# Kernel tuning notes

Measured on AMD Instinct MI355X. Metric: run time of the kernel, lower is better.

Reference implementation:

```python
import jax, jax.numpy as jnp
import numpy as np

N, L = 4096, 512

def setup_inputs() -> dict:
    key = jax.random.key(0)
    ks = jax.random.split(key, 12)
    def w(k, shape, fan_in):
        return jax.random.normal(k, shape, jnp.float32) / np.sqrt(fan_in)
    inp = {
        'samples': jax.random.normal(ks[0], (N, 1, L), jnp.float32),
        'samples_info': jax.random.randint(ks[1], (N, 2), 0, 2).astype(jnp.int64),
        'conv1_w': w(ks[2], (64, 1, 100), 100),
        'conv1_b': jnp.zeros((64,), jnp.float32),
        'conv2_w': w(ks[3], (128, 64, 5), 64 * 5),
        'conv2_b': jnp.zeros((128,), jnp.float32),
        'conv3_w': w(ks[4], (256, 128, 3), 128 * 3),
        'conv3_b': jnp.zeros((256,), jnp.float32),
        'fc_w': w(ks[5], (128, 256), 256),
        'fc_b': jnp.zeros((128,), jnp.float32),
        'bn_gamma': jnp.ones((128,), jnp.float32),
        'bn_beta': jnp.zeros((128,), jnp.float32),
        'bn_mean': jnp.zeros((128,), jnp.float32),
        'bn_var': jnp.ones((128,), jnp.float32),
    }
    return inp

def _conv1d(x, w, b, pad):
    # x: [N,C,L], w: [O,C,K]; torch padding='same' for k=100 pads (49,50)
    y = jax.lax.conv_general_dilated(x, w, window_strides=(1,), padding=[pad],
                                     dimension_numbers=('NCH', 'OIH', 'NCH'))
    return y + b[None, :, None]

def _maxpool2(x):
    n, c, l = x.shape
    return x.reshape(n, c, l // 2, 2).max(-1)

def reference(samples, samples_info, conv1_w, conv1_b, conv2_w, conv2_b,
              conv3_w, conv3_b, fc_w, fc_b, bn_gamma, bn_beta, bn_mean, bn_var):
    h = _maxpool2(jax.nn.relu(_conv1d(samples, conv1_w, conv1_b, (49, 50))))
    h = _maxpool2(jax.nn.relu(_conv1d(h, conv2_w, conv2_b, (2, 2))))
    h = _maxpool2(jax.nn.relu(_conv1d(h, conv3_w, conv3_b, (1, 1))))
    h = h.mean(-1)                                  # AdaptiveAvgPool1d(1)+Flatten -> [N,256]
    h = jax.nn.relu(h @ fc_w.T + fc_b)              # Linear 256->128
    z = bn_gamma * (h - bn_mean) * jax.lax.rsqrt(bn_var + 1e-5) + bn_beta  # BN (eval)
    # all-pairs euclidean distances via the cdist identity (replaces N^2 python loop)
    sq = jnp.sum(z * z, axis=-1)
    d2 = sq[:, None] + sq[None, :] - 2.0 * (z @ z.T)
    n = z.shape[0]
    offdiag = ~jnp.eye(n, dtype=bool)
    d = jnp.sqrt(jnp.where(offdiag, jnp.maximum(d2, 0.0), 1.0))
    writer = samples_info[:, 0]
    gen = samples_info[:, 1]
    y = ((writer[:, None] == writer[None, :]) & (gen[:, None] == 1) & (gen[None, :] == 1)).astype(z.dtype)
    cl = jnp.where(offdiag, y * d + (1.0 - y) * jax.nn.relu(1.0 - d), 0.0)
    return cl  # [N,N] contrastive loss per ordered pair (i!=j); diagonal masked to 0
```

## Files before the change

### kernel.cpp

```cpp
#include <hip/hip_runtime.h>
#include <math.h>

#define NS 4096

typedef _Float16 half8 __attribute__((ext_vector_type(8)));
typedef _Float16 half2v __attribute__((ext_vector_type(2)));
typedef float floatx16 __attribute__((ext_vector_type(16)));

#define P1T_OFF     0
#define P1T_STRIDE  72
#define P2T_OFF     9360
#define P2T_STRIDE  136
#define XC_OFF      9360
#define XC_STRIDE   648
#define SCR_OFF     1024
#define B1_OFF      18200
#define B2_OFF      18264
#define B3_OFF      18392
#define PR_OFF      18648
#define LDS_MAIN_FLOATS 19288

__global__ void prep_weights(const float* __restrict__ w1,
                             const float* __restrict__ w2,
                             const float* __restrict__ w3,
                             _Float16* __restrict__ w1p,
                             _Float16* __restrict__ w2p,
                             _Float16* __restrict__ w3p)
{
    int gid = blockIdx.x * 256 + threadIdx.x;
    if (gid < 8192) {
        int m = gid >> 7, k = gid & 127;
        w1p[gid] = (k < 100) ? (_Float16)w1[m * 100 + k] : (_Float16)0.f;
    } else if (gid < 49152) {
        int r = gid - 8192;
        int dk = r >> 13, rem = r & 8191;
        int m = rem >> 6, i = rem & 63;
        w2p[r] = (_Float16)w2[(m * 64 + i) * 5 + dk];
    } else if (gid < 147456) {
        int r = gid - 49152;
        int dk = r >> 15, rem = r & 32767;
        int m = rem >> 7, i = rem & 127;
        w3p[r] = (_Float16)w3[(m * 128 + i) * 3 + dk];
    }
}

__device__ __forceinline__ float dpp_rowsum16(float v) {
    int x;
    x = __builtin_amdgcn_update_dpp(0, __float_as_int(v), 0x111, 0xF, 0xF, true);
    v += __int_as_float(x);
    x = __builtin_amdgcn_update_dpp(0, __float_as_int(v), 0x112, 0xF, 0xF, true);
    v += __int_as_float(x);
    x = __builtin_amdgcn_update_dpp(0, __float_as_int(v), 0x114, 0xF, 0xF, true);
    v += __int_as_float(x);
    x = __builtin_amdgcn_update_dpp(0, __float_as_int(v), 0x118, 0xF, 0xF, true);
    v += __int_as_float(x);
    return v;
}


__global__ __launch_bounds__(512, 4)
void cnn_fused(const float* __restrict__ samples, const int* __restrict__ info,
               const _Float16* __restrict__ w1p,
               const _Float16* __restrict__ w2p,
               const _Float16* __restrict__ w3p,
               const float* __restrict__ b1, const float* __restrict__ b2,
               const float* __restrict__ b3,
               const float* __restrict__ fcw, const float* __restrict__ fcb,
               const float* __restrict__ gamma_, const float* __restrict__ beta_,
               const float* __restrict__ bnm, const float* __restrict__ bnv,
               _Float16* __restrict__ zh, float* __restrict__ sqout,
               int* __restrict__ uout)
{
    extern __shared__ float lds[];
    _Float16* p1T = (_Float16*)(lds + P1T_OFF);
    _Float16* p2T = (_Float16*)(lds + P2T_OFF);
    _Float16* xc  = (_Float16*)(lds + XC_OFF);

    const int n    = blockIdx.x;
    const int t    = threadIdx.x;
    const int lane = t & 63;
    const int wave = t >> 6;
    const int g    = lane >> 5;
    const int col  = lane & 31;

    {
        const float* sp = samples + n * 512;
        const int c = wave;
        for (int u = lane; u < XC_STRIDE; u += 64) {
            int src = u + c - 49;
            xc[c * XC_STRIDE + u] = (_Float16)((src >= 0 && src < 512) ? sp[src] : 0.f);
        }
    }
    if (t < 64)              lds[B1_OFF + t] = b1[t];
    if (t >= 64 && t < 192)  lds[B2_OFF + (t - 64)] = b2[t - 64];
    if (t >= 192 && t < 448) lds[B3_OFF + (t - 192)] = b3[t - 192];
    for (int i = t; i < 640; i += 512) {
        int k = i & 127;
        const float* p = (i < 128) ? fcb : (i < 256) ? gamma_ : (i < 384) ? beta_
                       : (i < 512) ? bnm : bnv;
        lds[PR_OFF + i] = p[k];
    }
    if (t < 144) {
        int rr = t / 36, c4 = t - rr * 36;
        int row = (rr < 2) ? rr : (256 + rr);
        lds[P1T_OFF + row * 36 + c4] = 0.f;
    }
    if (t == 0) uout[n] = (info[2 * n + 1] == 1) ? info[2 * n] : -1;
    __syncthreads();

    auto pool_store = [&](floatx16& acc, _Float16* dst) {
        float vm[16];
        #pragma unroll
        for (int r = 0; r < 16; ++r) {
            float v = fmaxf(acc[r], 0.f);
            vm[r] = fmaxf(v, __shfl_xor(v, 1));
        }
        if (!(lane & 1)) {
            #pragma unroll
            for (int rq = 0; rq < 4; ++rq) {
                half2v p0, p1;
                p0[0] = (_Float16)vm[4 * rq];     p0[1] = (_Float16)vm[4 * rq + 1];
                p1[0] = (_Float16)vm[4 * rq + 2]; p1[1] = (_Float16)vm[4 * rq + 3];
                *(half2v*)(dst + 8 * rq)     = p0;
                *(half2v*)(dst + 8 * rq + 2) = p1;
            }
        }
    };

    {
        const int mt   = wave >> 2;
        const int ntb1 = (wave & 3) * 4;
        half8 A[7];
        #pragma unroll
        for (int kb = 0; kb < 7; ++kb)
            A[kb] = *(const half8*)(w1p + (mt * 32 + col) * 128 + kb * 16 + g * 8);
        float4 bq[4];
        #pragma unroll
        for (int q4 = 0; q4 < 4; ++q4)
            bq[q4] = *(const float4*)&lds[B1_OFF + mt * 32 + 8 * q4 + 4 * g];
        #pragma unroll
        for (int s = 0; s < 4; ++s) {
            const int nt = ntb1 + s;
            const int nn = nt * 32 + col;
            const int c  = nn & 7;
            const _Float16* xcp = xc + c * XC_STRIDE + (nn - c) + g * 8;
            floatx16 a;
            #pragma unroll
            for (int q4 = 0; q4 < 4; ++q4) {
                a[4 * q4 + 0] = bq[q4].x; a[4 * q4 + 1] = bq[q4].y;
                a[4 * q4 + 2] = bq[q4].z; a[4 * q4 + 3] = bq[q4].w;
            }
            #pragma unroll
            for (int kb = 0; kb < 7; ++kb) {
                half8 B = *(const half8*)(xcp + kb * 16);
                a = __builtin_amdgcn_mfma_f32_32x32x16_f16(A[kb], B, a, 0, 0, 0);
            }
            const int P = 2 + nt * 16 + (col >> 1);
            pool_store(a, p1T + P * P1T_STRIDE + mt * 32 + 4 * g);
        }
    }
    __syncthreads();

    {
        if (t < 136) {
            int row = (t < 68) ? 0 : 129;
            int c4 = (t < 68) ? t : (t - 68);
            lds[P2T_OFF + row * 68 + c4] = 0.f;
        }
        const int mt  = wave & 3;
        const int ntb = (wave >> 2) * 4;
        floatx16 acc[4];
        #pragma unroll
        for (int q4 = 0; q4 < 4; ++q4) {
            float4 bq = *(const float4*)&lds[B2_OFF + mt * 32 + 8 * q4 + 4 * g];
            #pragma unroll
            for (int s = 0; s < 4; ++s) {
                acc[s][4 * q4 + 0] = bq.x; acc[s][4 * q4 + 1] = bq.y;
                acc[s][4 * q4 + 2] = bq.z; acc[s][4 * q4 + 3] = bq.w;
            }
        }
        half8 Ac[4], An[4];
        #pragma unroll
        for (int kb = 0; kb < 4; ++kb)
            Ac[kb] = *(const half8*)(w2p + (mt * 32 + col) * 64 + kb * 16 + g * 8);
        #pragma unroll 1
        for (int dk = 0; dk < 5; ++dk) {
            if (dk < 4) {
                #pragma unroll
                for (int kb = 0; kb < 4; ++kb)
                    An[kb] = *(const half8*)(w2p + ((dk + 1) * 128 + mt * 32 + col) * 64 + kb * 16 + g * 8);
            }
            #pragma unroll
            for (int s = 0; s < 4; ++s) {
                const int row = (ntb + s) * 32 + col + dk;
                const _Float16* bp = p1T + row * P1T_STRIDE + g * 8;
                #pragma unroll
                for (int kb = 0; kb < 4; ++kb) {
                    half8 B = *(const half8*)(bp + kb * 16);
                    acc[s] = __builtin_amdgcn_mfma_f32_32x32x16_f16(Ac[kb], B, acc[s], 0, 0, 0);
                }
            }
            if (dk < 4) {
                #pragma unroll
                for (int kb = 0; kb < 4; ++kb) Ac[kb] = An[kb];
            }
        }
        #pragma unroll
        for (int s = 0; s < 4; ++s) {
            const int P = 1 + (ntb + s) * 16 + (col >> 1);
            pool_store(acc[s], p2T + P * P2T_STRIDE + mt * 32 + 4 * g);
        }
    }
    __syncthreads();

    {
        const int mt = wave;
        floatx16 acc[4];
        #pragma unroll
        for (int q4 = 0; q4 < 4; ++q4) {
            float4 bq = *(const float4*)&lds[B3_OFF + mt * 32 + 8 * q4 + 4 * g];
            #pragma unroll
            for (int s = 0; s < 4; ++s) {
                acc[s][4 * q4 + 0] = bq.x; acc[s][4 * q4 + 1] = bq.y;
                acc[s][4 * q4 + 2] = bq.z; acc[s][4 * q4 + 3] = bq.w;
            }
        }
        #pragma unroll 1
        for (int dk = 0; dk < 3; ++dk) {
            half8 A[8];
            #pragma unroll
            for (int kb = 0; kb < 8; ++kb)
                A[kb] = *(const half8*)(w3p + (dk * 256 + mt * 32 + col) * 128 + kb * 16 + g * 8);
            #pragma unroll
            for (int s = 0; s < 4; ++s) {
                const int row = s * 32 + col + dk;
                const _Float16* bp = p2T + row * P2T_STRIDE + g * 8;
                #pragma unroll
                for (int kb = 0; kb < 8; ++kb) {
                    half8 B = *(const half8*)(bp + kb * 16);
                    acc[s] = __builtin_amdgcn_mfma_f32_32x32x16_f16(A[kb], B, acc[s], 0, 0, 0);
                }
            }
        }
        #pragma unroll
        for (int r = 0; r < 16; ++r) {
            float srow = 0.f;
            #pragma unroll
            for (int s = 0; s < 4; ++s) {
                float v = fmaxf(acc[s][r], 0.f);
                srow += fmaxf(v, __shfl_xor(v, 1));
            }
            float s16 = dpp_rowsum16(srow);
            float s32 = s16 + __shfl_xor(s16, 16);
            if ((lane & 31) == 15) {
                int ch = mt * 32 + (r & 3) + 8 * (r >> 2) + 4 * g;
                lds[SCR_OFF + ch] = s32 * (1.f / 128.f);
            }
        }
    }
    __syncthreads();

    {
        const float4 xv = *(const float4*)&lds[SCR_OFF + 4 * lane];
        #pragma unroll 1
        for (int ow = 0; ow < 16; ow += 4) {
            const int o0 = wave * 16 + ow;
            const float4 w0 = *(const float4*)&fcw[(o0 + 0) * 256 + 4 * lane];
            const float4 w1 = *(const float4*)&fcw[(o0 + 1) * 256 + 4 * lane];
            const float4 w2 = *(const float4*)&fcw[(o0 + 2) * 256 + 4 * lane];
            const float4 w3 = *(const float4*)&fcw[(o0 + 3) * 256 + 4 * lane];
            float s0 = w0.x * xv.x + w0.y * xv.y + w0.z * xv.z + w0.w * xv.w;
            float s1 = w1.x * xv.x + w1.y * xv.y + w1.z * xv.z + w1.w * xv.w;
            float s2 = w2.x * xv.x + w2.y * xv.y + w2.z * xv.z + w2.w * xv.w;
            float s3 = w3.x * xv.x + w3.y * xv.y + w3.z * xv.z + w3.w * xv.w;
            #pragma unroll
            for (int off = 32; off > 0; off >>= 1) {
                s0 += __shfl_down(s0, off);
                s1 += __shfl_down(s1, off);
                s2 += __shfl_down(s2, off);
                s3 += __shfl_down(s3, off);
            }
            if (lane == 0) {
                float4 o;
                o.x = fmaxf(s0 + lds[PR_OFF + o0 + 0], 0.f);
                o.y = fmaxf(s1 + lds[PR_OFF + o0 + 1], 0.f);
                o.z = fmaxf(s2 + lds[PR_OFF + o0 + 2], 0.f);
                o.w = fmaxf(s3 + lds[PR_OFF + o0 + 3], 0.f);
                *(float4*)&lds[SCR_OFF + 256 + o0] = o;
            }
        }
    }
    __syncthreads();

    if (t < 128) {
        float hv = lds[SCR_OFF + 256 + t];
        float zv = lds[PR_OFF + 128 + t] * (hv - lds[PR_OFF + 384 + t])
                   * (1.f / sqrtf(lds[PR_OFF + 512 + t] + 1e-5f)) + lds[PR_OFF + 256 + t];
        _Float16 zq = (_Float16)zv;
        zh[(size_t)n * 128 + t] = zq;
        float zqf = (float)zq;
        lds[SCR_OFF + 384 + t] = zqf * zqf;
    }
    __syncthreads();
    if (t < 64) {
        float s = lds[SCR_OFF + 384 + t] + lds[SCR_OFF + 384 + 64 + t];
        #pragma unroll
        for (int off = 32; off > 0; off >>= 1) s += __shfl_down(s, off);
        if (t == 0) sqout[n] = s;
    }
}

#define PW_STRIDE 136
#define PW_LDS_BYTES (2 * 128 * PW_STRIDE * 2)

__global__ __launch_bounds__(256, 2)
void pairwise_mfma(const _Float16* __restrict__ zh, const float* __restrict__ sq,
                   const int* __restrict__ u, float* __restrict__ out)
{
    extern __shared__ float ldsf[];
    _Float16* at = (_Float16*)ldsf;
    _Float16* bt = at + 128 * PW_STRIDE;
    const int t = threadIdx.x;
    const int i0 = blockIdx.y * 128;
    const int j0 = blockIdx.x * 128;

    #pragma unroll
    for (int r4 = 0; r4 < 8; ++r4) {
        int idx = t + 256 * r4;
        int row = idx >> 4, c8 = (idx & 15) * 8;
        *(half8*)(at + row * PW_STRIDE + c8) = *(const half8*)(zh + (size_t)(i0 + row) * 128 + c8);
        *(half8*)(bt + row * PW_STRIDE + c8) = *(const half8*)(zh + (size_t)(j0 + row) * 128 + c8);
    }
    __syncthreads();

    const int lane = t & 63, wave = t >> 6;
    const int g = lane >> 5, col = lane & 31;
    const int ib = (wave & 1) * 64, jb = (wave >> 1) * 64;

    half8 A[2][8];
    #pragma unroll
    for (int mt = 0; mt < 2; ++mt)
        #pragma unroll
        for (int kb = 0; kb < 8; ++kb)
            A[mt][kb] = *(const half8*)(at + (ib + mt * 32 + col) * PW_STRIDE + kb * 16 + g * 8);

    floatx16 acc[2][2];
    #pragma unroll
    for (int a = 0; a < 2; ++a)
        #pragma unroll
        for (int b = 0; b < 2; ++b)
            #pragma unroll
            for (int r = 0; r < 16; ++r) acc[a][b][r] = 0.f;

    #pragma unroll
    for (int nt = 0; nt < 2; ++nt)
        #pragma unroll
        for (int kb = 0; kb < 8; ++kb) {
            half8 B = *(const half8*)(bt + (jb + nt * 32 + col) * PW_STRIDE + kb * 16 + g * 8);
            acc[0][nt] = __builtin_amdgcn_mfma_f32_32x32x16_f16(A[0][kb], B, acc[0][nt], 0, 0, 0);
            acc[1][nt] = __builtin_amdgcn_mfma_f32_32x32x16_f16(A[1][kb], B, acc[1][nt], 0, 0, 0);
        }

    #pragma unroll
    for (int nt = 0; nt < 2; ++nt) {
        const int j = j0 + jb + nt * 32 + col;
        const float sqj = sq[j];
        const int uj = u[j];
        #pragma unroll
        for (int mt = 0; mt < 2; ++mt) {
            #pragma unroll
            for (int r = 0; r < 16; ++r) {
                const int i = i0 + ib + mt * 32 + (r & 3) + 8 * (r >> 2) + 4 * g;
                float res;
                if (i == j) {
                    res = 0.f;
                } else {
                    float d2 = sq[i] + sqj - 2.f * acc[mt][nt][r];
                    float d = sqrtf(fmaxf(d2, 0.f));
                    int ui = u[i];
                    res = (ui == uj && ui >= 0) ? d : fmaxf(1.f - d, 0.f);
                }
                out[(size_t)i * 4096 + j] = res;
            }
        }
    }
}

extern "C" void kernel_launch(void* const* d_in, const int* in_sizes, int n_in,
                              void* d_out, int out_size, void* d_ws, size_t ws_size,
                              hipStream_t stream)
{
    const float* samples = (const float*)d_in[0];
    const int*   info    = (const int*)d_in[1];
    const float* w1  = (const float*)d_in[2];
    const float* b1  = (const float*)d_in[3];
    const float* w2  = (const float*)d_in[4];
    const float* b2  = (const float*)d_in[5];
    const float* w3  = (const float*)d_in[6];
    const float* b3  = (const float*)d_in[7];
    const float* fcw = (const float*)d_in[8];
    const float* fcb = (const float*)d_in[9];
    const float* g   = (const float*)d_in[10];
    const float* be  = (const float*)d_in[11];
    const float* bm  = (const float*)d_in[12];
    const float* bv  = (const float*)d_in[13];
    float* out = (float*)d_out;

    _Float16* zhws = (_Float16*)d_ws;
    float*    sqws = (float*)((char*)d_ws + (1 << 20));
    int*      uws  = (int*)((char*)d_ws + (1 << 20) + 16384);
    _Float16* wp   = (_Float16*)((char*)d_ws + (1 << 20) + 32768);
    _Float16* w1p = wp;
    _Float16* w2p = wp + 8192;
    _Float16* w3p = wp + 49152;

    hipLaunchKernelGGL(prep_weights, dim3(576), dim3(256), 0, stream,
                       w1, w2, w3, w1p, w2p, w3p);

    hipLaunchKernelGGL(cnn_fused, dim3(NS), dim3(512),
                       LDS_MAIN_FLOATS * sizeof(float), stream,
                       samples, info, w1p, w2p, w3p, b1, b2, b3, fcw, fcb,
                       g, be, bm, bv, zhws, sqws, uws);

    hipLaunchKernelGGL(pairwise_mfma, dim3(32, 32), dim3(256),
                       PW_LDS_BYTES, stream,
                       zhws, sqws, uws, out);
}
```

Measured before the change: 425.4 us.

## Software-pipeline conv MFMA loops, fuse FC/BN epilogue, slim pairwise LDS

The three conv stages are restructured into fully unrolled loops that double/triple-buffer A and B fragments, so loads for step i+1 are issued while MFMAs for step i run, and accumulators are shared across the N tiles. The FC output, BN and fp16 quantization plus the squared norm are fused into the FC reduction lane, which removes two barriers and the LDS round trips between them. The pairwise kernel now reads the A operand straight from global memory instead of staging it in LDS, halving LDS use and raising launch_bounds occupancy to 4. In exchange it uses more registers and makes uncoalesced global reads in the pairwise kernel.

```diff
diff --git a/kernel.cpp b/kernel.cpp
--- a/kernel.cpp
+++ b/kernel.cpp
@@ -130,33 +130,47 @@
     {
         const int mt   = wave >> 2;
         const int ntb1 = (wave & 3) * 4;
-        half8 A[7];
-        #pragma unroll
-        for (int kb = 0; kb < 7; ++kb)
-            A[kb] = *(const half8*)(w1p + (mt * 32 + col) * 128 + kb * 16 + g * 8);
-        float4 bq[4];
-        #pragma unroll
-        for (int q4 = 0; q4 < 4; ++q4)
-            bq[q4] = *(const float4*)&lds[B1_OFF + mt * 32 + 8 * q4 + 4 * g];
+        const _Float16* ap = w1p + (mt * 32 + col) * 128 + g * 8;
+        const _Float16* bps[4];
         #pragma unroll
         for (int s = 0; s < 4; ++s) {
             const int nt = ntb1 + s;
             const int nn = nt * 32 + col;
             const int c  = nn & 7;
-            const _Float16* xcp = xc + c * XC_STRIDE + (nn - c) + g * 8;
-            floatx16 a;
-            #pragma unroll
-            for (int q4 = 0; q4 < 4; ++q4) {
-                a[4 * q4 + 0] = bq[q4].x; a[4 * q4 + 1] = bq[q4].y;
-                a[4 * q4 + 2] = bq[q4].z; a[4 * q4 + 3] = bq[q4].w;
-            }
-            #pragma unroll
-            for (int kb = 0; kb < 7; ++kb) {
-                half8 B = *(const half8*)(xcp + kb * 16);
-                a = __builtin_amdgcn_mfma_f32_32x32x16_f16(A[kb], B, a, 0, 0, 0);
-            }
-            const int P = 2 + nt * 16 + (col >> 1);
-            pool_store(a, p1T + P * P1T_STRIDE + mt * 32 + 4 * g);
+            bps[s] = xc + c * XC_STRIDE + (nn - c) + g * 8;
+        }
+        floatx16 acc[4];
+        #pragma unroll
+        for (int q4 = 0; q4 < 4; ++q4) {
+            float4 bq = *(const float4*)&lds[B1_OFF + mt * 32 + 8 * q4 + 4 * g];
+            #pragma unroll
+            for (int s = 0; s < 4; ++s) {
+                acc[s][4 * q4 + 0] = bq.x; acc[s][4 * q4 + 1] = bq.y;
+                acc[s][4 * q4 + 2] = bq.z; acc[s][4 * q4 + 3] = bq.w;
+            }
+        }
+        half8 Aa[3], Bb[2][4];
+        Aa[0] = *(const half8*)(ap);
+        Aa[1] = *(const half8*)(ap + 16);
+        #pragma unroll
+        for (int s = 0; s < 4; ++s) Bb[0][s] = *(const half8*)(bps[s]);
+        #pragma unroll
+        for (int i = 0; i < 7; ++i) {
+            if (i < 5)
+                Aa[(i + 2) % 3] = *(const half8*)(ap + (i + 2) * 16);
+            if (i < 6) {
+                #pragma unroll
+                for (int s = 0; s < 4; ++s)
+                    Bb[(i + 1) & 1][s] = *(const half8*)(bps[s] + (i + 1) * 16);
+            }
+            #pragma unroll
+            for (int s = 0; s < 4; ++s)
+                acc[s] = __builtin_amdgcn_mfma_f32_32x32x16_f16(Aa[i % 3], Bb[i & 1][s], acc[s], 0, 0, 0);
+        }
+        #pragma unroll
+        for (int s = 0; s < 4; ++s) {
+            const int P = 2 + (ntb1 + s) * 16 + (col >> 1);
+            pool_store(acc[s], p1T + P * P1T_STRIDE + mt * 32 + 4 * g);
         }
     }
     __syncthreads();
@@ -169,6 +183,11 @@
         }
         const int mt  = wave & 3;
         const int ntb = (wave >> 2) * 4;
+        const _Float16* ap = w2p + (mt * 32 + col) * 64 + g * 8;
+        const _Float16* bps[4];
+        #pragma unroll
+        for (int s = 0; s < 4; ++s)
+            bps[s] = p1T + ((ntb + s) * 32 + col) * P1T_STRIDE + g * 8;
         floatx16 acc[4];
         #pragma unroll
         for (int q4 = 0; q4 < 4; ++q4) {
@@ -179,31 +198,26 @@
                 acc[s][4 * q4 + 2] = bq.z; acc[s][4 * q4 + 3] = bq.w;
             }
         }
-        half8 Ac[4], An[4];
-        #pragma unroll
-        for (int kb = 0; kb < 4; ++kb)
-            Ac[kb] = *(const half8*)(w2p + (mt * 32 + col) * 64 + kb * 16 + g * 8);
-        #pragma unroll 1
-        for (int dk = 0; dk < 5; ++dk) {
-            if (dk < 4) {
+        half8 Aa[3], Bb[2][4];
+        Aa[0] = *(const half8*)(ap);
+        Aa[1] = *(const half8*)(ap + 16);
+        #pragma unroll
+        for (int s = 0; s < 4; ++s) Bb[0][s] = *(const half8*)(bps[s]);
+        #pragma unroll
+        for (int i = 0; i < 20; ++i) {
+            if (i < 18) {
+                const int j = i + 2, dkj = j >> 2, kbj = j & 3;
+                Aa[(i + 2) % 3] = *(const half8*)(ap + dkj * 8192 + kbj * 16);
+            }
+            if (i < 19) {
+                const int j = i + 1, dkj = j >> 2, kbj = j & 3;
                 #pragma unroll
-                for (int kb = 0; kb < 4; ++kb)
-                    An[kb] = *(const half8*)(w2p + ((dk + 1) * 128 + mt * 32 + col) * 64 + kb * 16 + g * 8);
-            }
-            #pragma unroll
-            for (int s = 0; s < 4; ++s) {
-                const int row = (ntb + s) * 32 + col + dk;
-                const _Float16* bp = p1T + row * P1T_STRIDE + g * 8;
-                #pragma unroll
-                for (int kb = 0; kb < 4; ++kb) {
-                    half8 B = *(const half8*)(bp + kb * 16);
-                    acc[s] = __builtin_amdgcn_mfma_f32_32x32x16_f16(Ac[kb], B, acc[s], 0, 0, 0);
-                }
-            }
-            if (dk < 4) {
-                #pragma unroll
-                for (int kb = 0; kb < 4; ++kb) Ac[kb] = An[kb];
-            }
+                for (int s = 0; s < 4; ++s)
+                    Bb[j & 1][s] = *(const half8*)(bps[s] + dkj * P1T_STRIDE + kbj * 16);
+            }
+            #pragma unroll
+            for (int s = 0; s < 4; ++s)
+                acc[s] = __builtin_amdgcn_mfma_f32_32x32x16_f16(Aa[i % 3], Bb[i & 1][s], acc[s], 0, 0, 0);
         }
         #pragma unroll
         for (int s = 0; s < 4; ++s) {
@@ -215,6 +229,11 @@
 
     {
         const int mt = wave;
+        const _Float16* ap = w3p + (mt * 32 + col) * 128 + g * 8;
+        const _Float16* bps[4];
+        #pragma unroll
+        for (int s = 0; s < 4; ++s)
+            bps[s] = p2T + (s * 32 + col) * P2T_STRIDE + g * 8;
         floatx16 acc[4];
         #pragma unroll
         for (int q4 = 0; q4 < 4; ++q4) {
@@ -225,22 +244,26 @@
                 acc[s][4 * q4 + 2] = bq.z; acc[s][4 * q4 + 3] = bq.w;
             }
         }
-        #pragma unroll 1
-        for (int dk = 0; dk < 3; ++dk) {
-            half8 A[8];
-            #pragma unroll
-            for (int kb = 0; kb < 8; ++kb)
-                A[kb] = *(const half8*)(w3p + (dk * 256 + mt * 32 + col) * 128 + kb * 16 + g * 8);
-            #pragma unroll
-            for (int s = 0; s < 4; ++s) {
-                const int row = s * 32 + col + dk;
-                const _Float16* bp = p2T + row * P2T_STRIDE + g * 8;
+        half8 Aa[3], Bb[2][4];
+        Aa[0] = *(const half8*)(ap);
+        Aa[1] = *(const half8*)(ap + 16);
+        #pragma unroll
+        for (int s = 0; s < 4; ++s) Bb[0][s] = *(const half8*)(bps[s]);
+        #pragma unroll
+        for (int i = 0; i < 24; ++i) {
+            if (i < 22) {
+                const int j = i + 2, dkj = j >> 3, kbj = j & 7;
+                Aa[(i + 2) % 3] = *(const half8*)(ap + dkj * 32768 + kbj * 16);
+            }
+            if (i < 23) {
+                const int j = i + 1, dkj = j >> 3, kbj = j & 7;
                 #pragma unroll
-                for (int kb = 0; kb < 8; ++kb) {
-                    half8 B = *(const half8*)(bp + kb * 16);
-                    acc[s] = __builtin_amdgcn_mfma_f32_32x32x16_f16(A[kb], B, acc[s], 0, 0, 0);
-                }
-            }
+                for (int s = 0; s < 4; ++s)
+                    Bb[j & 1][s] = *(const half8*)(bps[s] + dkj * P2T_STRIDE + kbj * 16);
+            }
+            #pragma unroll
+            for (int s = 0; s < 4; ++s)
+                acc[s] = __builtin_amdgcn_mfma_f32_32x32x16_f16(Aa[i % 3], Bb[i & 1][s], acc[s], 0, 0, 0);
         }
         #pragma unroll
         for (int r = 0; r < 16; ++r) {
@@ -262,6 +285,7 @@
 
     {
         const float4 xv = *(const float4*)&lds[SCR_OFF + 4 * lane];
+        float sqpart = 0.f;
         #pragma unroll 1
         for (int ow = 0; ow < 16; ow += 4) {
             const int o0 = wave * 16 + ow;
@@ -281,45 +305,43 @@
                 s3 += __shfl_down(s3, off);
             }
             if (lane == 0) {
-                float4 o;
-                o.x = fmaxf(s0 + lds[PR_OFF + o0 + 0], 0.f);
-                o.y = fmaxf(s1 + lds[PR_OFF + o0 + 1], 0.f);
-                o.z = fmaxf(s2 + lds[PR_OFF + o0 + 2], 0.f);
-                o.w = fmaxf(s3 + lds[PR_OFF + o0 + 3], 0.f);
-                *(float4*)&lds[SCR_OFF + 256 + o0] = o;
-            }
-        }
-    }
-    __syncthreads();
-
-    if (t < 128) {
-        float hv = lds[SCR_OFF + 256 + t];
-        float zv = lds[PR_OFF + 128 + t] * (hv - lds[PR_OFF + 384 + t])
-                   * (1.f / sqrtf(lds[PR_OFF + 512 + t] + 1e-5f)) + lds[PR_OFF + 256 + t];
-        _Float16 zq = (_Float16)zv;
-        zh[(size_t)n * 128 + t] = zq;
-        float zqf = (float)zq;
-        lds[SCR_OFF + 384 + t] = zqf * zqf;
-    }
-    __syncthreads();
-    if (t < 64) {
-        float s = lds[SCR_OFF + 384 + t] + lds[SCR_OFF + 384 + 64 + t];
-        #pragma unroll
-        for (int off = 32; off > 0; off >>= 1) s += __shfl_down(s, off);
-        if (t == 0) sqout[n] = s;
+                float sv[4] = {s0, s1, s2, s3};
+                half2v zp0, zp1;
+                #pragma unroll
+                for (int k = 0; k < 4; ++k) {
+                    float hv = fmaxf(sv[k] + lds[PR_OFF + o0 + k], 0.f);
+                    float zv = lds[PR_OFF + 128 + o0 + k] * (hv - lds[PR_OFF + 384 + o0 + k])
+                             * (1.f / sqrtf(lds[PR_OFF + 512 + o0 + k] + 1e-5f))
+                             + lds[PR_OFF + 256 + o0 + k];
+                    _Float16 zq = (_Float16)zv;
+                    if (k < 2) zp0[k] = zq; else zp1[k - 2] = zq;
+                    float zqf = (float)zq;
+                    sqpart += zqf * zqf;
+                }
+                *(half2v*)(zh + (size_t)n * 128 + o0)     = zp0;
+                *(half2v*)(zh + (size_t)n * 128 + o0 + 2) = zp1;
+            }
+        }
+        if (lane == 0) lds[SCR_OFF + 256 + wave] = sqpart;
+    }
+    __syncthreads();
+    if (t == 0) {
+        float s = 0.f;
+        #pragma unroll
+        for (int w = 0; w < 8; ++w) s += lds[SCR_OFF + 256 + w];
+        sqout[n] = s;
     }
 }
 
 #define PW_STRIDE 136
-#define PW_LDS_BYTES (2 * 128 * PW_STRIDE * 2)
-
-__global__ __launch_bounds__(256, 2)
+#define PW_LDS_BYTES (128 * PW_STRIDE * 2)
+
+__global__ __launch_bounds__(256, 4)
 void pairwise_mfma(const _Float16* __restrict__ zh, const float* __restrict__ sq,
                    const int* __restrict__ u, float* __restrict__ out)
 {
     extern __shared__ float ldsf[];
-    _Float16* at = (_Float16*)ldsf;
-    _Float16* bt = at + 128 * PW_STRIDE;
+    _Float16* bt = (_Float16*)ldsf;
     const int t = threadIdx.x;
     const int i0 = blockIdx.y * 128;
     const int j0 = blockIdx.x * 128;
@@ -328,7 +350,6 @@
     for (int r4 = 0; r4 < 8; ++r4) {
         int idx = t + 256 * r4;
         int row = idx >> 4, c8 = (idx & 15) * 8;
-        *(half8*)(at + row * PW_STRIDE + c8) = *(const half8*)(zh + (size_t)(i0 + row) * 128 + c8);
         *(half8*)(bt + row * PW_STRIDE + c8) = *(const half8*)(zh + (size_t)(j0 + row) * 128 + c8);
     }
     __syncthreads();
@@ -337,12 +358,10 @@
     const int g = lane >> 5, col = lane & 31;
     const int ib = (wave & 1) * 64, jb = (wave >> 1) * 64;
 
-    half8 A[2][8];
-    #pragma unroll
-    for (int mt = 0; mt < 2; ++mt)
-        #pragma unroll
-        for (int kb = 0; kb < 8; ++kb)
-            A[mt][kb] = *(const half8*)(at + (ib + mt * 32 + col) * PW_STRIDE + kb * 16 + g * 8);
+    const _Float16* ap0 = zh + (size_t)(i0 + ib + col) * 128 + g * 8;
+    const _Float16* ap1 = zh + (size_t)(i0 + ib + 32 + col) * 128 + g * 8;
+    const _Float16* bp0 = bt + (jb + col) * PW_STRIDE + g * 8;
+    const _Float16* bp1 = bt + (jb + 32 + col) * PW_STRIDE + g * 8;
 
     floatx16 acc[2][2];
     #pragma unroll
@@ -352,14 +371,24 @@
             #pragma unroll
             for (int r = 0; r < 16; ++r) acc[a][b][r] = 0.f;
 
+    half8 A0[2], A1[2], B0[2], B1[2];
+    A0[0] = *(const half8*)(ap0);
+    A1[0] = *(const half8*)(ap1);
+    B0[0] = *(const half8*)(bp0);
+    B1[0] = *(const half8*)(bp1);
     #pragma unroll
-    for (int nt = 0; nt < 2; ++nt)
-        #pragma unroll
-        for (int kb = 0; kb < 8; ++kb) {
-            half8 B = *(const half8*)(bt + (jb + nt * 32 + col) * PW_STRIDE + kb * 16 + g * 8);
-            acc[0][nt] = __builtin_amdgcn_mfma_f32_32x32x16_f16(A[0][kb], B, acc[0][nt], 0, 0, 0);
-            acc[1][nt] = __builtin_amdgcn_mfma_f32_32x32x16_f16(A[1][kb], B, acc[1][nt], 0, 0, 0);
-        }
+    for (int kb = 0; kb < 8; ++kb) {
+        if (kb < 7) {
+            A0[(kb + 1) & 1] = *(const half8*)(ap0 + (kb + 1) * 16);
+            A1[(kb + 1) & 1] = *(const half8*)(ap1 + (kb + 1) * 16);
+            B0[(kb + 1) & 1] = *(const half8*)(bp0 + (kb + 1) * 16);
+            B1[(kb + 1) & 1] = *(const half8*)(bp1 + (kb + 1) * 16);
+        }
+        acc[0][0] = __builtin_amdgcn_mfma_f32_32x32x16_f16(A0[kb & 1], B0[kb & 1], acc[0][0], 0, 0, 0);
+        acc[0][1] = __builtin_amdgcn_mfma_f32_32x32x16_f16(A0[kb & 1], B1[kb & 1], acc[0][1], 0, 0, 0);
+        acc[1][0] = __builtin_amdgcn_mfma_f32_32x32x16_f16(A1[kb & 1], B0[kb & 1], acc[1][0], 0, 0, 0);
+        acc[1][1] = __builtin_amdgcn_mfma_f32_32x32x16_f16(A1[kb & 1], B1[kb & 1], acc[1][1], 0, 0, 0);
+    }
 
     #pragma unroll
     for (int nt = 0; nt < 2; ++nt) {
```

After: 428.1 us. About the same (+0.6%).
